# Kernel tuning notes

Measured on AMD Instinct MI355X. Metric: run time of the kernel, lower is better.

The kernel has to match this reference:

```python
import jax, jax.numpy as jnp
import numpy as np
from jax import lax

B, CEN, CDE, H, W = 4, 256, 256, 64, 64   # de is (B,CDE,H,W); en is (B,CEN,2H,2W)
EMB, K, SCALE = 64, 5, 2
DN = ('NCHW', 'OIHW', 'NCHW')


def conv2d(x, w, b=None, pad=0):
    y = lax.conv_general_dilated(x, w, (1, 1), [(pad, pad), (pad, pad)], dimension_numbers=DN)
    return y if b is None else y + b[None, :, None, None]


def up2(x):
    # F.interpolate(scale_factor=2) default mode='nearest'
    return jnp.repeat(jnp.repeat(x, 2, axis=2), 2, axis=3)


def carafe(de, kernels, k, scale):
    # de: (B,C,H,W); kernels: (B,k*k,H*scale,W*scale), softmax-normalized over dim 1
    b, c, h, w = de.shape
    pad = k // 2
    dep = jnp.pad(de, ((0, 0), (0, 0), (pad, pad), (pad, pad)))
    # (B, C, k*k, H, W): all k*k shifted views of de (zero-padded borders)
    patches = jnp.stack([dep[:, :, dy:dy + h, dx:dx + w]
                         for dy in range(k) for dx in range(k)], axis=2)
    # each output pixel (i,j) reuses the window at source (i//scale, j//scale)
    ker = kernels.reshape(b, k * k, h, scale, w, scale)
    out = jnp.einsum('bkhxwy,bckhw->bchxwy', ker, patches)
    return out.reshape(b, c, h * scale, w * scale)


def xavier_uniform(key, shape):
    fan_out = shape[0] * shape[2] * shape[3]
    fan_in = shape[1] * shape[2] * shape[3]
    limit = float(np.sqrt(6.0 / (fan_in + fan_out)))
    return jax.random.uniform(key, shape, jnp.float32, -limit, limit)


def setup_inputs() -> dict:
    key = jax.random.key(0)
    ks = jax.random.split(key, 7)
    return {
        'en': jax.random.normal(ks[0], (B, CEN, 2 * H, 2 * W), jnp.float32),
        'de': jax.random.normal(ks[1], (B, CDE, H, W), jnp.float32),
        'w_gate': xavier_uniform(ks[2], (1, CDE, 1, 1)),
        'b_gate': jnp.zeros((1,), jnp.float32),
        'w_cen': xavier_uniform(ks[3], (EMB, CEN, 1, 1)),
        'b_cen': jnp.zeros((EMB,), jnp.float32),
        'w_cde': xavier_uniform(ks[4], (EMB, CDE, 1, 1)),
        'w_ce': xavier_uniform(ks[5], (K * K, EMB, 3, 3)),
        'b_ce': jnp.zeros((K * K,), jnp.float32),
    }


def reference(en, de, w_gate, b_gate, w_cen, b_cen, w_cde, w_ce, b_ce):
    # GateGenerator: sigmoid(interpolate(conv1x1(de), x2))
    gate = jax.nn.sigmoid(up2(conv2d(de, w_gate, b_gate)))
    # SemiShift: shared 3x3 content encoder on compressed en and upsampled compressed de
    enc = conv2d(en, w_cen, b_cen)
    dec = conv2d(de, w_cde)          # no bias
    logits = conv2d(enc, w_ce, b_ce, pad=1) + up2(conv2d(dec, w_ce, b_ce, pad=1))
    kernels = jax.nn.softmax(logits, axis=1)
    return gate * en + (1.0 - gate) * carafe(de, kernels, K, SCALE)
```

## Files before the change

kernel.cpp:

```cpp
#include <hip/hip_runtime.h>
#include <math.h>

#define BB 4
#define C 256
#define H 64
#define W 64
#define HW 4096
#define HO 128
#define WO 128
#define HWO 16384
#define EMB 64

typedef __bf16 bf16x8 __attribute__((ext_vector_type(8)));
typedef __bf16 bf16x4 __attribute__((ext_vector_type(4)));
typedef float  f32x4  __attribute__((ext_vector_type(4)));

__device__ __forceinline__ f32x4 mfma16(bf16x8 a, bf16x8 b, f32x4 c) {
    return __builtin_amdgcn_mfma_f32_16x16x32_bf16(a, b, c, 0, 0, 0);
}

__global__ void k_prep2(const float* __restrict__ w_cen,
                        const float* __restrict__ w_cde,
                        const float* __restrict__ w_gate,
                        const float* __restrict__ w_ce,
                        __bf16* __restrict__ wbf_cen,
                        __bf16* __restrict__ wdec5,
                        __bf16* __restrict__ w3) {
    for (int idx = blockIdx.x * blockDim.x + threadIdx.x; idx < 16384;
         idx += gridDim.x * blockDim.x)
        wbf_cen[idx] = (__bf16)w_cen[idx];
    for (int idx = blockIdx.x * blockDim.x + threadIdx.x; idx < 20480;
         idx += gridDim.x * blockDim.x) {
        int c = idx & 255, m = (idx >> 8) & 15;
        float v;
        if (idx < 16384) v = w_cde[idx];
        else             v = (m == 0) ? w_gate[c] : 0.f;
        wdec5[idx] = (__bf16)v;
    }
    for (int idx = blockIdx.x * blockDim.x + threadIdx.x; idx < 18432;
         idx += gridDim.x * blockDim.x) {
        int e = idx & 63;
        int m = (idx >> 6) & 15;
        int mt = (idx >> 10) & 1;
        int tap = idx >> 11;
        int q = mt * 16 + m;
        int dy = tap / 3, dx = tap % 3;
        w3[idx] = (q < 25) ? (__bf16)w_ce[((q * EMB + e) * 3 + dy) * 3 + dx]
                           : (__bf16)0.0f;
    }
}

__global__ __launch_bounds__(256) void k_gemm1(
        const float* __restrict__ en, const float* __restrict__ de,
        const __bf16* __restrict__ wbf_cen, const __bf16* __restrict__ wdec5,
        const float* __restrict__ b_cen, const float* __restrict__ b_gate,
        __bf16* __restrict__ enc_t, __bf16* __restrict__ dec_t,
        float* __restrict__ gate_lr) {
    __shared__ float xs[2][32][136];
    int t = threadIdx.x;
    int w = t >> 6, lane = t & 63;
    int n = lane & 15, q = lane >> 4;
    bool isenc = blockIdx.x < 512;
    const float* X; const __bf16* Wt; __bf16* Y; int plane, px0, b;
    if (isenc) {
        int blk = blockIdx.x; b = blk >> 7; px0 = (blk & 127) << 7;
        X = en + (size_t)b * C * HWO; plane = HWO; Wt = wbf_cen;
        Y = enc_t + (size_t)b * HWO * EMB;
    } else {
        int blk = blockIdx.x - 512; b = blk >> 5; px0 = (blk & 31) << 7;
        X = de + (size_t)b * C * HW; plane = HW; Wt = wdec5;
        Y = dec_t + (size_t)b * HW * EMB;
    }
    int scc = t >> 5;
    int sp4 = (t & 31) << 2;
    float4 pre[4];
    #pragma unroll
    for (int i = 0; i < 4; i++)
        pre[i] = *(const float4*)(X + (size_t)(i * 8 + scc) * plane + px0 + sp4);
    #pragma unroll
    for (int i = 0; i < 4; i++)
        *(float4*)(&xs[0][i * 8 + scc][sp4]) = pre[i];
    __syncthreads();

    f32x4 acc[4][2] = {};
    f32x4 accg[2] = {};
    for (int kc = 0; kc < 8; kc++) {
        int cur = kc & 1;
        if (kc < 7) {
            int c1 = (kc + 1) * 32;
            #pragma unroll
            for (int i = 0; i < 4; i++)
                pre[i] = *(const float4*)(X + (size_t)(c1 + i * 8 + scc) * plane
                                          + px0 + sp4);
        }
        int c0 = kc * 32;
        bf16x8 af[4];
        #pragma unroll
        for (int mt = 0; mt < 4; mt++)
            af[mt] = *(const bf16x8*)(Wt + (size_t)(mt * 16 + n) * C + c0 + q * 8);
        bf16x8 bv[2];
        #pragma unroll
        for (int nt = 0; nt < 2; nt++) {
            int px = w * 32 + nt * 16 + n;
            #pragma unroll
            for (int j = 0; j < 8; j++)
                bv[nt][j] = (__bf16)xs[cur][q * 8 + j][px];
        }
        #pragma unroll
        for (int mt = 0; mt < 4; mt++) {
            acc[mt][0] = mfma16(af[mt], bv[0], acc[mt][0]);
            acc[mt][1] = mfma16(af[mt], bv[1], acc[mt][1]);
        }
        if (!isenc) {
            bf16x8 ag = *(const bf16x8*)(Wt + (size_t)(64 + n) * C + c0 + q * 8);
            accg[0] = mfma16(ag, bv[0], accg[0]);
            accg[1] = mfma16(ag, bv[1], accg[1]);
        }
        if (kc < 7) {
            #pragma unroll
            for (int i = 0; i < 4; i++)
                *(float4*)(&xs[cur ^ 1][i * 8 + scc][sp4]) = pre[i];
        }
        __syncthreads();
    }

    #pragma unroll
    for (int nt = 0; nt < 2; nt++) {
        int gpx = px0 + w * 32 + nt * 16 + n;
        #pragma unroll
        for (int mt = 0; mt < 4; mt++) {
            int e0 = mt * 16 + q * 4;
            bf16x4 ov;
            #pragma unroll
            for (int r = 0; r < 4; r++) {
                float bias = isenc ? b_cen[e0 + r] : 0.f;
                ov[r] = (__bf16)(acc[mt][nt][r] + bias);
            }
            *(bf16x4*)(Y + (size_t)gpx * EMB + e0) = ov;
        }
        if (!isenc && q == 0)
            gate_lr[b * HW + gpx] =
                1.f / (1.f + __expf(-(accg[nt][0] + b_gate[0])));
    }
}

__global__ __launch_bounds__(256) void k_conv3m(
        const __bf16* __restrict__ enc_t, const __bf16* __restrict__ dec_t,
        const __bf16* __restrict__ w3, const float* __restrict__ b_ce,
        float* __restrict__ tmp1, float* __restrict__ tmp2) {
    __shared__ __bf16 sfr[8 * 3 * 66 * 8];
    int t = threadIdx.x;
    int w = t >> 6, lane = t & 63;
    int n = lane & 15, q = lane >> 4;
    bool hi = blockIdx.x < 1024;
    const __bf16* src; float* dst; int b, y, width, plane, x0;
    if (hi) {
        int blk = blockIdx.x; b = blk >> 8; int r = blk & 255;
        y = r >> 1; x0 = (r & 1) * 64;
        width = WO; plane = HWO;
        src = enc_t + (size_t)b * HWO * EMB; dst = tmp1;
    } else {
        int blk = blockIdx.x - 1024; b = blk >> 6; y = blk & 63; x0 = 0;
        width = W; plane = HW;
        src = dec_t + (size_t)b * HW * EMB; dst = tmp2;
    }
    bf16x8 zf;
    #pragma unroll
    for (int j = 0; j < 8; j++) zf[j] = (__bf16)0.0f;
    for (int idx = t; idx < 1584; idx += 256) {
        int f = idx & 7;
        int rem = idx >> 3;
        int xloc = rem % 66, row = rem / 66;
        int yy = y + row - 1, xg = x0 - 1 + xloc;
        bf16x8 v = zf;
        if ((unsigned)yy < (unsigned)width && (unsigned)xg < (unsigned)width)
            v = *(const bf16x8*)(src + ((size_t)yy * width + xg) * EMB + f * 8);
        *(bf16x8*)(sfr + (((f * 3) + row) * 66 + xloc) * 8) = v;
    }
    __syncthreads();

    int x = w * 16 + n;
    f32x4 acc[2] = {};
    #pragma unroll
    for (int row = 0; row < 3; row++) {
        #pragma unroll
        for (int dx = 0; dx < 3; dx++) {
            int tap = row * 3 + dx;
            #pragma unroll
            for (int kc = 0; kc < 2; kc++) {
                bf16x8 bv = *(const bf16x8*)(
                    sfr + ((((kc * 4 + q) * 3) + row) * 66 + x + dx) * 8);
                #pragma unroll
                for (int mt = 0; mt < 2; mt++) {
                    bf16x8 av = *(const bf16x8*)(
                        w3 + ((tap * 2 + mt) * 16 + n) * EMB + kc * 32 + q * 8);
                    acc[mt] = mfma16(av, bv, acc[mt]);
                }
            }
        }
    }
    #pragma unroll
    for (int mt = 0; mt < 2; mt++) {
        #pragma unroll
        for (int r = 0; r < 4; r++) {
            int m = mt * 16 + q * 4 + r;
            if (m < 25)
                dst[((size_t)(b * 25 + m)) * plane + y * width + x0 + x] =
                    acc[mt][r] + b_ce[m];
        }
    }
}

#define NCH 16
__global__ __launch_bounds__(256) void k_final(
        const float* __restrict__ en, const float* __restrict__ de,
        const float* __restrict__ tmp1, const float* __restrict__ tmp2,
        const float* __restrict__ gate_lr, float* __restrict__ out) {
    __shared__ float sde[NCH][8][36];
    int t = threadIdx.x;
    int x0 = (blockIdx.x & 1) * 32, y0 = (blockIdx.x >> 1) * 4;
    int c0 = blockIdx.y * NCH;
    int b = blockIdx.z;

    const float* dbase = de + ((size_t)b * C + c0) * HW;
    for (int idx = t; idx < NCH * 288; idx += 256) {
        int c = idx / 288, rem = idx % 288;
        int row = rem / 36, col = rem % 36;
        int yy = y0 - 2 + row, xx = x0 - 2 + col;
        float v = 0.f;
        if ((unsigned)yy < (unsigned)H && (unsigned)xx < (unsigned)W)
            v = dbase[(size_t)c * HW + yy * W + xx];
        sde[c][row][col] = v;
    }

    int tx = t & 31;
    int tyr = t >> 5;
    int ty = tyr >> 1, r = tyr & 1;
    int yl = y0 + ty, xl = x0 + tx;
    int hrow = 2 * yl + r;
    int p0 = hrow * WO + 2 * xl;
    int pl = yl * W + xl;

    float l0[25], l1[25];
    const float* t1 = tmp1 + (((size_t)b * 25) << 14) + p0;
    const float* t2 = tmp2 + (((size_t)b * 25) << 12) + pl;
    float mx0 = -1e30f, mx1 = -1e30f;
    #pragma unroll
    for (int q = 0; q < 25; q++) {
        float2 a = *(const float2*)(t1 + ((size_t)q << 14));
        float cq = t2[(size_t)q << 12];
        l0[q] = a.x + cq; l1[q] = a.y + cq;
        mx0 = fmaxf(mx0, l0[q]); mx1 = fmaxf(mx1, l1[q]);
    }
    float s0 = 0.f, s1 = 0.f;
    #pragma unroll
    for (int q = 0; q < 25; q++) {
        l0[q] = __expf(l0[q] - mx0); s0 += l0[q];
        l1[q] = __expf(l1[q] - mx1); s1 += l1[q];
    }
    float g = gate_lr[b * HW + pl];
    float gi0 = (1.f - g) / s0;
    float gi1 = (1.f - g) / s1;
    __syncthreads();

    const float* ebase = en + ((size_t)b * C + c0) * HWO + p0;
    float* obase = out + ((size_t)b * C + c0) * HWO + p0;
    #pragma unroll 2
    for (int c = 0; c < NCH; c++) {
        float a0 = 0.f, a1 = 0.f;
        #pragma unroll
        for (int dy = 0; dy < 5; dy++) {
            #pragma unroll
            for (int dx = 0; dx < 5; dx++) {
                float v = sde[c][ty + dy][tx + dx];
                int k = dy * 5 + dx;
                a0 += l0[k] * v;
                a1 += l1[k] * v;
            }
        }
        size_t cc = (size_t)c * HWO;
        float2 e = *(const float2*)(ebase + cc);
        float2 o;
        o.x = g * e.x + gi0 * a0;
        o.y = g * e.y + gi1 * a1;
        *(float2*)(obase + cc) = o;
    }
}

extern "C" void kernel_launch(void* const* d_in, const int* in_sizes, int n_in,
                              void* d_out, int out_size, void* d_ws, size_t ws_size,
                              hipStream_t stream) {
    const float* en     = (const float*)d_in[0];
    const float* de     = (const float*)d_in[1];
    const float* w_gate = (const float*)d_in[2];
    const float* b_gate = (const float*)d_in[3];
    const float* w_cen  = (const float*)d_in[4];
    const float* b_cen  = (const float*)d_in[5];
    const float* w_cde  = (const float*)d_in[6];
    const float* w_ce   = (const float*)d_in[7];
    const float* b_ce   = (const float*)d_in[8];
    float* out = (float*)d_out;

    __bf16* wsb     = (__bf16*)d_ws;
    __bf16* wbf_cen = wsb;
    __bf16* wdec5   = wbf_cen + 16384;
    __bf16* w3      = wdec5 + 20480;
    __bf16* enc_t   = w3 + 18432;
    __bf16* dec_t   = enc_t + 4194304;
    float* wsf     = (float*)((char*)d_ws + (size_t)(16384 + 20480 + 18432
                              + 4194304 + 1048576) * 2);
    float* tmp1    = wsf;
    float* tmp2    = tmp1 + 1638400;
    float* gate_lr = tmp2 + 409600;

    k_prep2<<<80, 256, 0, stream>>>(w_cen, w_cde, w_gate, w_ce,
                                    wbf_cen, wdec5, w3);
    k_gemm1<<<640, 256, 0, stream>>>(en, de, wbf_cen, wdec5, b_cen, b_gate,
                                     enc_t, dec_t, gate_lr);
    k_conv3m<<<1280, 256, 0, stream>>>(enc_t, dec_t, w3, b_ce, tmp1, tmp2);
    k_final<<<dim3(32, 16, 4), 256, 0, stream>>>(en, de, tmp1, tmp2,
                                                 gate_lr, out);
}
```

Measured before the change: 215.0 us.

## Drop LDS staging in 1x1 GEMM and load activations directly into registers

The 1x1-conv GEMM kernel no longer stages activations through double-buffered shared memory with block barriers. Each lane now loads its 8 channel values straight from global memory into registers, with a register-level prefetch of the next channel chunk. Each block covers 64 pixels instead of 128, so the grid doubles to 1280 blocks. This removes LDS traffic and syncs and adds parallelism, at the cost of scalar strided global loads that each read only 16 consecutive floats per row (less coalesced) and weight fragments reused over fewer pixels.

```diff
diff --git a/kernel.cpp b/kernel.cpp
--- a/kernel.cpp
+++ b/kernel.cpp
@@ -56,92 +56,69 @@
         const float* __restrict__ b_cen, const float* __restrict__ b_gate,
         __bf16* __restrict__ enc_t, __bf16* __restrict__ dec_t,
         float* __restrict__ gate_lr) {
-    __shared__ float xs[2][32][136];
     int t = threadIdx.x;
     int w = t >> 6, lane = t & 63;
     int n = lane & 15, q = lane >> 4;
-    bool isenc = blockIdx.x < 512;
+    bool isenc = blockIdx.x < 1024;
     const float* X; const __bf16* Wt; __bf16* Y; int plane, px0, b;
     if (isenc) {
-        int blk = blockIdx.x; b = blk >> 7; px0 = (blk & 127) << 7;
+        int blk = blockIdx.x; b = blk >> 8; px0 = (blk & 255) << 6;
         X = en + (size_t)b * C * HWO; plane = HWO; Wt = wbf_cen;
         Y = enc_t + (size_t)b * HWO * EMB;
     } else {
-        int blk = blockIdx.x - 512; b = blk >> 5; px0 = (blk & 31) << 7;
+        int blk = blockIdx.x - 1024; b = blk >> 6; px0 = (blk & 63) << 6;
         X = de + (size_t)b * C * HW; plane = HW; Wt = wdec5;
         Y = dec_t + (size_t)b * HW * EMB;
     }
-    int scc = t >> 5;
-    int sp4 = (t & 31) << 2;
-    float4 pre[4];
-    #pragma unroll
-    for (int i = 0; i < 4; i++)
-        pre[i] = *(const float4*)(X + (size_t)(i * 8 + scc) * plane + px0 + sp4);
-    #pragma unroll
-    for (int i = 0; i < 4; i++)
-        *(float4*)(&xs[0][i * 8 + scc][sp4]) = pre[i];
-    __syncthreads();
-
-    f32x4 acc[4][2] = {};
-    f32x4 accg[2] = {};
+    int px = px0 + w * 16 + n;
+    const float* Xp = X + (size_t)(q * 8) * plane + px;
+
+    f32x4 acc[4] = {};
+    f32x4 accg = {};
+    float cur[8];
+    #pragma unroll
+    for (int j = 0; j < 8; j++) cur[j] = Xp[(size_t)j * plane];
+
     for (int kc = 0; kc < 8; kc++) {
-        int cur = kc & 1;
+        float nxt[8];
         if (kc < 7) {
-            int c1 = (kc + 1) * 32;
+            const float* Xn = Xp + (size_t)((kc + 1) * 32) * plane;
             #pragma unroll
-            for (int i = 0; i < 4; i++)
-                pre[i] = *(const float4*)(X + (size_t)(c1 + i * 8 + scc) * plane
-                                          + px0 + sp4);
-        }
+            for (int j = 0; j < 8; j++) nxt[j] = Xn[(size_t)j * plane];
+        }
+        bf16x8 bv;
+        #pragma unroll
+        for (int j = 0; j < 8; j++) bv[j] = (__bf16)cur[j];
         int c0 = kc * 32;
-        bf16x8 af[4];
-        #pragma unroll
-        for (int mt = 0; mt < 4; mt++)
-            af[mt] = *(const bf16x8*)(Wt + (size_t)(mt * 16 + n) * C + c0 + q * 8);
-        bf16x8 bv[2];
-        #pragma unroll
-        for (int nt = 0; nt < 2; nt++) {
-            int px = w * 32 + nt * 16 + n;
-            #pragma unroll
-            for (int j = 0; j < 8; j++)
-                bv[nt][j] = (__bf16)xs[cur][q * 8 + j][px];
-        }
         #pragma unroll
         for (int mt = 0; mt < 4; mt++) {
-            acc[mt][0] = mfma16(af[mt], bv[0], acc[mt][0]);
-            acc[mt][1] = mfma16(af[mt], bv[1], acc[mt][1]);
+            bf16x8 af = *(const bf16x8*)(Wt + (size_t)(mt * 16 + n) * C
+                                         + c0 + q * 8);
+            acc[mt] = mfma16(af, bv, acc[mt]);
         }
         if (!isenc) {
             bf16x8 ag = *(const bf16x8*)(Wt + (size_t)(64 + n) * C + c0 + q * 8);
-            accg[0] = mfma16(ag, bv[0], accg[0]);
-            accg[1] = mfma16(ag, bv[1], accg[1]);
+            accg = mfma16(ag, bv, accg);
         }
         if (kc < 7) {
             #pragma unroll
-            for (int i = 0; i < 4; i++)
-                *(float4*)(&xs[cur ^ 1][i * 8 + scc][sp4]) = pre[i];
-        }
-        __syncthreads();
-    }
-
-    #pragma unroll
-    for (int nt = 0; nt < 2; nt++) {
-        int gpx = px0 + w * 32 + nt * 16 + n;
-        #pragma unroll
-        for (int mt = 0; mt < 4; mt++) {
-            int e0 = mt * 16 + q * 4;
-            bf16x4 ov;
-            #pragma unroll
-            for (int r = 0; r < 4; r++) {
-                float bias = isenc ? b_cen[e0 + r] : 0.f;
-                ov[r] = (__bf16)(acc[mt][nt][r] + bias);
-            }
-            *(bf16x4*)(Y + (size_t)gpx * EMB + e0) = ov;
-        }
-        if (!isenc && q == 0)
-            gate_lr[b * HW + gpx] =
-                1.f / (1.f + __expf(-(accg[nt][0] + b_gate[0])));
-    }
+            for (int j = 0; j < 8; j++) cur[j] = nxt[j];
+        }
+    }
+
+    #pragma unroll
+    for (int mt = 0; mt < 4; mt++) {
+        int e0 = mt * 16 + q * 4;
+        bf16x4 ov;
+        #pragma unroll
+        for (int r = 0; r < 4; r++) {
+            float bias = isenc ? b_cen[e0 + r] : 0.f;
+            ov[r] = (__bf16)(acc[mt][r] + bias);
+        }
+        *(bf16x4*)(Y + (size_t)px * EMB + e0) = ov;
+    }
+    if (!isenc && q == 0)
+        gate_lr[b * HW + px] = 1.f / (1.f + __expf(-(accg[0] + b_gate[0])));
 }
 
 __global__ __launch_bounds__(256) void k_conv3m(
@@ -315,8 +292,8 @@
 
     k_prep2<<<80, 256, 0, stream>>>(w_cen, w_cde, w_gate, w_ce,
                                     wbf_cen, wdec5, w3);
-    k_gemm1<<<640, 256, 0, stream>>>(en, de, wbf_cen, wdec5, b_cen, b_gate,
-                                     enc_t, dec_t, gate_lr);
+    k_gemm1<<<1280, 256, 0, stream>>>(en, de, wbf_cen, wdec5, b_cen, b_gate,
+                                      enc_t, dec_t, gate_lr);
     k_conv3m<<<1280, 256, 0, stream>>>(enc_t, dec_t, w3, b_ce, tmp1, tmp2);
     k_final<<<dim3(32, 16, 4), 256, 0, stream>>>(en, de, tmp1, tmp2,
                                                  gate_lr, out);
```

Measured after the change: 222.9 us. +3.7%, slower.
